# Performance work log

Measured on AMD Instinct MI355X. Metric: run time of the kernel, lower is better.

Reference implementation:

```python
import jax, jax.numpy as jnp
import numpy as np
import math

B, S, E, H = 2, 2048, 1024, 16
D = E // H  # head_dim = 64


def setup_inputs() -> dict:
    key = jax.random.key(0)
    ks = jax.random.split(key, 5)
    scale_p = 1.0 / math.sqrt(D)
    return {
        "x": jax.random.normal(ks[0], (B, S, E), dtype=jnp.float32),
        "Wq": jax.random.normal(ks[1], (D, D), dtype=jnp.float32) * scale_p,
        "Wk": jax.random.normal(ks[2], (D, D), dtype=jnp.float32) * scale_p,
        "Wv": jax.random.normal(ks[3], (D, D), dtype=jnp.float32) * scale_p,
        "W_out": jax.random.normal(ks[4], (E, E), dtype=jnp.float32) * (1.0 / math.sqrt(E)),
        "b_out": jnp.zeros((E,), dtype=jnp.float32),
    }


def reference(x, Wq, Wk, Wv, W_out, b_out):
    b, s, e = x.shape
    xh = x.reshape(b, s, H, D)  # [B,S,H,D]
    # per-head linear projections (torch Linear: y = x @ W.T), weights shared across heads
    q = jnp.einsum("bshd,ed->bshe", xh, Wq)
    k = jnp.einsum("bshd,ed->bshe", xh, Wk)
    v = jnp.einsum("bshd,ed->bshe", xh, Wv)
    # scaled dot-product attention, scale = sqrt(embed_dim) per tutorial-style impl
    energy = jnp.einsum("bqhd,bkhd->bhqk", q, k) / jnp.sqrt(jnp.float32(e))
    attn = jax.nn.softmax(energy, axis=-1)  # [B,H,S,S]
    out = jnp.einsum("bhqk,bkhd->bqhd", attn, v).reshape(b, s, e)
    return out @ W_out.T + b_out
```

## Files before the change

### kernel.cpp

```cpp
#include <hip/hip_runtime.h>
#include <math.h>

#define BB 2
#define SS 2048
#define EE 1024
#define HH 16
#define DD 64
constexpr int NROWS = BB * SS * HH;
constexpr float SCALE_Q = 1.4426950408889634f / 32.0f;

typedef __attribute__((ext_vector_type(8))) short bf16x8;
typedef __attribute__((ext_vector_type(4))) float f32x4;
typedef __attribute__((ext_vector_type(16))) float f32x16;
typedef __attribute__((ext_vector_type(4))) unsigned u32x4;

__device__ inline ushort f2bf(float f) {
  unsigned u = __builtin_bit_cast(unsigned, f);
  u += 0x7fffu + ((u >> 16) & 1u);
  return (ushort)(u >> 16);
}

__device__ inline unsigned cvt_pk(float lo, float hi) {
  unsigned r;
  asm("v_cvt_pk_bf16_f32 %0, %1, %2" : "=v"(r) : "v"(lo), "v"(hi));
  return r;
}

__global__ __launch_bounds__(256) void wqkv_cvt(
    const float* __restrict__ Wq, const float* __restrict__ Wk,
    const float* __restrict__ Wv, ushort* __restrict__ o) {
  int i = blockIdx.x * 256 + threadIdx.x;
  int t = i >> 12, j = i & 4095;
  const float* W = (t == 0) ? Wq : ((t == 1) ? Wk : Wv);
  o[i] = f2bf(W[j]);
}

__global__ __launch_bounds__(256) void qkv_mfma(
    const float* __restrict__ x, const ushort* __restrict__ wqkv,
    ushort* __restrict__ qo, ushort* __restrict__ ko, ushort* __restrict__ vto) {
  __shared__ __align__(16) ushort Xs[128 * 72];
  __shared__ __align__(16) ushort Ws[3][64 * 72];
  const int tid = threadIdx.x, w = tid >> 6, l = tid & 63;
  const int g = l >> 4, c = l & 15;
  const int s0 = blockIdx.x * 128, h = blockIdx.y, b = blockIdx.z;

  for (int i = tid; i < 1536; i += 256) {
    int t = i >> 9, j = i & 511;
    int r = j >> 3, e0 = (j & 7) * 8;
    *(bf16x8*)&Ws[t][r * 72 + e0] = *(const bf16x8*)&wqkv[t * 4096 + r * 64 + e0];
  }
  for (int i = tid; i < 2048; i += 256) {
    int r = i >> 4, c4 = (i & 15) * 4;
    float4 xv = *(const float4*)&x[(((size_t)b * SS + s0 + r) * HH + h) * DD + c4];
    uint2 pk;
    pk.x = cvt_pk(xv.x, xv.y);
    pk.y = cvt_pk(xv.z, xv.w);
    *(uint2*)&Xs[r * 72 + c4] = pk;
  }
  __syncthreads();

  bf16x8 a_[2][2];
#pragma unroll
  for (int rf = 0; rf < 2; ++rf) {
    a_[rf][0] = *(bf16x8*)&Xs[(w * 32 + rf * 16 + c) * 72 + g * 8];
    a_[rf][1] = *(bf16x8*)&Xs[(w * 32 + rf * 16 + c) * 72 + 32 + g * 8];
  }

#pragma unroll
  for (int t = 0; t < 2; ++t) {
    ushort* out = (t == 0) ? qo : ko;
    const float sc = (t == 0) ? SCALE_Q : 1.0f;
#pragma unroll
    for (int ct = 0; ct < 4; ++ct) {
      bf16x8 b0 = *(bf16x8*)&Ws[t][(ct * 16 + c) * 72 + g * 8];
      bf16x8 b1 = *(bf16x8*)&Ws[t][(ct * 16 + c) * 72 + 32 + g * 8];
#pragma unroll
      for (int rf = 0; rf < 2; ++rf) {
        f32x4 acc = (f32x4){0.f, 0.f, 0.f, 0.f};
        acc = __builtin_amdgcn_mfma_f32_16x16x32_bf16(a_[rf][0], b0, acc, 0, 0, 0);
        acc = __builtin_amdgcn_mfma_f32_16x16x32_bf16(a_[rf][1], b1, acc, 0, 0, 0);
#pragma unroll
        for (int r = 0; r < 4; ++r) {
          int srow = w * 32 + rf * 16 + g * 4 + r;
          out[(((size_t)b * SS + s0 + srow) * HH + h) * DD + ct * 16 + c] =
              f2bf(acc[r] * sc);
        }
      }
    }
  }
#pragma unroll
  for (int ct = 0; ct < 4; ++ct) {
    bf16x8 b0 = *(bf16x8*)&Ws[2][(ct * 16 + c) * 72 + g * 8];
    bf16x8 b1 = *(bf16x8*)&Ws[2][(ct * 16 + c) * 72 + 32 + g * 8];
#pragma unroll
    for (int rf = 0; rf < 2; ++rf) {
      f32x4 acc = (f32x4){0.f, 0.f, 0.f, 0.f};
      acc = __builtin_amdgcn_mfma_f32_16x16x32_bf16(a_[rf][0], b0, acc, 0, 0, 0);
      acc = __builtin_amdgcn_mfma_f32_16x16x32_bf16(a_[rf][1], b1, acc, 0, 0, 0);
      uint2 pk;
      pk.x = cvt_pk(acc[0], acc[1]);
      pk.y = cvt_pk(acc[2], acc[3]);
      int d = ct * 16 + c;
      int srow = w * 32 + rf * 16 + g * 4;
      *(uint2*)&vto[(((size_t)b * HH + h) * DD + d) * SS + s0 + srow] = pk;
    }
  }
}

__global__ __launch_bounds__(256) void wcvt(const float* __restrict__ w,
                                            ushort* __restrict__ o) {
  int i = (blockIdx.x * 256 + threadIdx.x) * 8;
  bf16x8 t;
#pragma unroll
  for (int j = 0; j < 8; ++j) t[j] = (short)f2bf(w[i + j]);
  *(bf16x8*)&o[i] = t;
}

__global__ __launch_bounds__(256) void attn_mfma(
    const ushort* __restrict__ q, const ushort* __restrict__ k,
    const ushort* __restrict__ vt, ushort* __restrict__ o) {
  __shared__ __align__(16) ushort Ks[2][64 * 72];
  __shared__ __align__(16) ushort Vts[2][64 * 72];
  const int tid = threadIdx.x, w = tid >> 6, l = tid & 63;
  const int lq = l & 31, h2 = l >> 5;
  const int work = ((blockIdx.x & 7) << 6) | (blockIdx.x >> 3);
  const int qt = work & 15, hb = work >> 4;
  const int h = hb & 15, b = hb >> 4;
  const int q0 = qt * 128;

  const size_t bh_qk = (size_t)b * SS * EE + h * DD;
  const size_t bh_vt = (size_t)b * SS * EE + h * (DD * SS);

  const int sr0 = tid >> 3;
  const int se0 = (tid & 7) * 8;
  const int krow0 = (sr0 & 19) | ((sr0 & 4) << 1) | ((sr0 & 8) >> 1);

  {
    bf16x8 kr0 = *(const bf16x8*)&k[bh_qk + (size_t)sr0 * EE + se0];
    bf16x8 kr1 = *(const bf16x8*)&k[bh_qk + (size_t)(sr0 + 32) * EE + se0];
    bf16x8 vr0 = *(const bf16x8*)&vt[bh_vt + (size_t)sr0 * SS + se0];
    bf16x8 vr1 = *(const bf16x8*)&vt[bh_vt + (size_t)(sr0 + 32) * SS + se0];
    *(bf16x8*)&Ks[0][krow0 * 72 + se0] = kr0;
    *(bf16x8*)&Ks[0][(krow0 + 32) * 72 + se0] = kr1;
    *(bf16x8*)&Vts[0][sr0 * 72 + se0] = vr0;
    *(bf16x8*)&Vts[0][(sr0 + 32) * 72 + se0] = vr1;
  }

  bf16x8 aq[4];
#pragma unroll
  for (int db = 0; db < 4; ++db)
    aq[db] = *(const bf16x8*)&q[bh_qk +
        (size_t)(q0 + w * 32 + lq) * EE + db * 16 + h2 * 8];

  f32x16 accO[2];
  float lacc = 0.f;
#pragma unroll
  for (int ct = 0; ct < 2; ++ct)
#pragma unroll
    for (int r = 0; r < 16; ++r) accO[ct][r] = 0.f;

  __syncthreads();

  for (int t = 0; t < 32; ++t) {
    const int cur = t & 1;
    bf16x8 kr0, kr1, vr0, vr1;
    if (t < 31) {
      const size_t kb2 = bh_qk + (size_t)((t + 1) * 64) * EE;
      kr0 = *(const bf16x8*)&k[kb2 + (size_t)sr0 * EE + se0];
      kr1 = *(const bf16x8*)&k[kb2 + (size_t)(sr0 + 32) * EE + se0];
      const size_t vb2 = bh_vt + (t + 1) * 64;
      vr0 = *(const bf16x8*)&vt[vb2 + (size_t)sr0 * SS + se0];
      vr1 = *(const bf16x8*)&vt[vb2 + (size_t)(sr0 + 32) * SS + se0];
    }

    f32x16 s[2];
    __builtin_amdgcn_s_setprio(1);
#pragma unroll
    for (int kb = 0; kb < 2; ++kb) {
      f32x16 acc;
#pragma unroll
      for (int r = 0; r < 16; ++r) acc[r] = 0.f;
#pragma unroll
      for (int db = 0; db < 4; ++db) {
        bf16x8 ka = *(bf16x8*)&Ks[cur][(kb * 32 + lq) * 72 + db * 16 + h2 * 8];
        acc = __builtin_amdgcn_mfma_f32_32x32x16_bf16(ka, aq[db], acc, 0, 0, 0);
      }
      s[kb] = acc;
    }
    __builtin_amdgcn_s_setprio(0);

    u32x4 pwv[2][2];
#pragma unroll
    for (int kb = 0; kb < 2; ++kb)
#pragma unroll
      for (int t16 = 0; t16 < 2; ++t16)
#pragma unroll
        for (int j2 = 0; j2 < 4; ++j2) {
          float pa = __builtin_amdgcn_exp2f(s[kb][t16 * 8 + j2 * 2]);
          float pb = __builtin_amdgcn_exp2f(s[kb][t16 * 8 + j2 * 2 + 1]);
          lacc += pa + pb;
          pwv[kb][t16][j2] = cvt_pk(pa, pb);
        }

    __builtin_amdgcn_s_setprio(1);
#pragma unroll
    for (int ct = 0; ct < 2; ++ct) {
#pragma unroll
      for (int kb = 0; kb < 2; ++kb)
#pragma unroll
        for (int t16 = 0; t16 < 2; ++t16) {
          bf16x8 va = *(bf16x8*)&Vts[cur][(ct * 32 + lq) * 72 +
                                          kb * 32 + t16 * 16 + h2 * 8];
          accO[ct] = __builtin_amdgcn_mfma_f32_32x32x16_bf16(
              va, __builtin_bit_cast(bf16x8, pwv[kb][t16]), accO[ct], 0, 0, 0);
        }
    }
    __builtin_amdgcn_s_setprio(0);

    if (t < 31) {
      const int nxt = cur ^ 1;
      *(bf16x8*)&Ks[nxt][krow0 * 72 + se0] = kr0;
      *(bf16x8*)&Ks[nxt][(krow0 + 32) * 72 + se0] = kr1;
      *(bf16x8*)&Vts[nxt][sr0 * 72 + se0] = vr0;
      *(bf16x8*)&Vts[nxt][(sr0 + 32) * 72 + se0] = vr1;
    }
    __syncthreads();
  }

  {
    float tsum = lacc + __shfl_xor(lacc, 32, 64);
    float inv = 1.f / tsum;
    size_t row = (size_t)b * SS + q0 + w * 32 + lq;
#pragma unroll
    for (int ct = 0; ct < 2; ++ct)
#pragma unroll
      for (int rq = 0; rq < 4; ++rq) {
        uint2 pk;
        pk.x = cvt_pk(accO[ct][rq * 4 + 0] * inv, accO[ct][rq * 4 + 1] * inv);
        pk.y = cvt_pk(accO[ct][rq * 4 + 2] * inv, accO[ct][rq * 4 + 3] * inv);
        *(uint2*)&o[row * EE + h * DD + ct * 32 + rq * 8 + h2 * 4] = pk;
      }
  }
}

__global__ __launch_bounds__(256) void out_proj_mfma(
    const ushort* __restrict__ a, const ushort* __restrict__ wo,
    const float* __restrict__ bias, float* __restrict__ y) {
  __shared__ __align__(16) ushort As[2][128 * 72];
  __shared__ __align__(16) ushort Ws[2][64 * 72];
  const int tid = threadIdx.x, w = tid >> 6, l = tid & 63;
  const int g = l >> 4, c = l & 15;
  const int m0 = blockIdx.x * 128, n0 = blockIdx.y * 64;
  const int sr = tid >> 3, se = (tid & 7) * 8;

  f32x4 acc[2][4];
#pragma unroll
  for (int mf = 0; mf < 2; ++mf)
#pragma unroll
    for (int ct = 0; ct < 4; ++ct) acc[mf][ct] = (f32x4){0.f, 0.f, 0.f, 0.f};

  {
#pragma unroll
    for (int j = 0; j < 4; ++j) {
      int r = sr + j * 32;
      *(bf16x8*)&As[0][r * 72 + se] = *(const bf16x8*)&a[(size_t)(m0 + r) * EE + se];
    }
#pragma unroll
    for (int j = 0; j < 2; ++j) {
      int r = sr + j * 32;
      *(bf16x8*)&Ws[0][r * 72 + se] = *(const bf16x8*)&wo[(size_t)(n0 + r) * EE + se];
    }
  }
  __syncthreads();

  for (int t = 0; t < 16; ++t) {
    const int cur = t & 1;
    bf16x8 Arg[4], Brg[2];
    if (t < 15) {
      const int k0 = (t + 1) * 64;
#pragma unroll
      for (int j = 0; j < 4; ++j) {
        int r = sr + j * 32;
        Arg[j] = *(const bf16x8*)&a[(size_t)(m0 + r) * EE + k0 + se];
      }
#pragma unroll
      for (int j = 0; j < 2; ++j) {
        int r = sr + j * 32;
        Brg[j] = *(const bf16x8*)&wo[(size_t)(n0 + r) * EE + k0 + se];
      }
    }

    bf16x8 af[2][2];
#pragma unroll
    for (int mf = 0; mf < 2; ++mf) {
      af[mf][0] = *(bf16x8*)&As[cur][(w * 32 + mf * 16 + c) * 72 + g * 8];
      af[mf][1] = *(bf16x8*)&As[cur][(w * 32 + mf * 16 + c) * 72 + 32 + g * 8];
    }
    __builtin_amdgcn_s_setprio(1);
#pragma unroll
    for (int ct = 0; ct < 4; ++ct) {
      bf16x8 b0 = *(bf16x8*)&Ws[cur][(ct * 16 + c) * 72 + g * 8];
      bf16x8 b1 = *(bf16x8*)&Ws[cur][(ct * 16 + c) * 72 + 32 + g * 8];
#pragma unroll
      for (int mf = 0; mf < 2; ++mf) {
        acc[mf][ct] = __builtin_amdgcn_mfma_f32_16x16x32_bf16(af[mf][0], b0, acc[mf][ct], 0, 0, 0);
        acc[mf][ct] = __builtin_amdgcn_mfma_f32_16x16x32_bf16(af[mf][1], b1, acc[mf][ct], 0, 0, 0);
      }
    }
    __builtin_amdgcn_s_setprio(0);

    if (t < 15) {
      const int nxt = cur ^ 1;
#pragma unroll
      for (int j = 0; j < 4; ++j) {
        int r = sr + j * 32;
        *(bf16x8*)&As[nxt][r * 72 + se] = Arg[j];
      }
#pragma unroll
      for (int j = 0; j < 2; ++j) {
        int r = sr + j * 32;
        *(bf16x8*)&Ws[nxt][r * 72 + se] = Brg[j];
      }
    }
    __syncthreads();
  }

#pragma unroll
  for (int ct = 0; ct < 4; ++ct) {
    float bv = bias[n0 + ct * 16 + c];
#pragma unroll
    for (int mf = 0; mf < 2; ++mf)
#pragma unroll
      for (int r = 0; r < 4; ++r)
        y[(size_t)(m0 + w * 32 + mf * 16 + g * 4 + r) * EE + n0 + ct * 16 + c] =
            acc[mf][ct][r] + bv;
  }
}

extern "C" void kernel_launch(void* const* d_in, const int* in_sizes, int n_in,
                              void* d_out, int out_size, void* d_ws,
                              size_t ws_size, hipStream_t stream) {
  const float* x = (const float*)d_in[0];
  const float* Wq = (const float*)d_in[1];
  const float* Wk = (const float*)d_in[2];
  const float* Wv = (const float*)d_in[3];
  const float* Wo = (const float*)d_in[4];
  const float* bo = (const float*)d_in[5];
  float* out = (float*)d_out;

  const size_t per = (size_t)NROWS * 64;
  ushort* qb = (ushort*)d_ws;
  ushort* kb = qb + per;
  ushort* vtb = kb + per;
  ushort* aob = vtb + per;
  ushort* wob = aob + per;
  ushort* wqkvb = wob + 1024 * 1024;

  wqkv_cvt<<<48, 256, 0, stream>>>(Wq, Wk, Wv, wqkvb);
  wcvt<<<512, 256, 0, stream>>>(Wo, wob);
  qkv_mfma<<<dim3(16, 16, 2), 256, 0, stream>>>(x, wqkvb, qb, kb, vtb);
  attn_mfma<<<512, 256, 0, stream>>>(qb, kb, vtb, aob);
  out_proj_mfma<<<dim3(32, 16), 256, 0, stream>>>(aob, wob, bo, out);
}
```

Baseline: 89.75 us.

## Split attention over two key halves with a separate combine kernel

The attention kernel now splits the 2048 keys into two halves handled by separate blocks, doubling the grid to 1024 blocks. Each block writes unnormalized fp32 partial outputs and row sums to workspace instead of a normalized bf16 result. A new combine kernel adds the two partials, divides by the summed row totals and writes the bf16 attention output. This is meant to raise occupancy and latency hiding on the CUs. The cost is a round trip of a large fp32 intermediate through memory plus one extra kernel launch.

```diff
diff --git a/kernel.cpp b/kernel.cpp
--- a/kernel.cpp
+++ b/kernel.cpp
@@ -118,28 +118,34 @@
 
 __global__ __launch_bounds__(256) void attn_mfma(
     const ushort* __restrict__ q, const ushort* __restrict__ k,
-    const ushort* __restrict__ vt, ushort* __restrict__ o) {
+    const ushort* __restrict__ vt, float* __restrict__ pO,
+    float* __restrict__ lsum) {
   __shared__ __align__(16) ushort Ks[2][64 * 72];
   __shared__ __align__(16) ushort Vts[2][64 * 72];
   const int tid = threadIdx.x, w = tid >> 6, l = tid & 63;
   const int lq = l & 31, h2 = l >> 5;
-  const int work = ((blockIdx.x & 7) << 6) | (blockIdx.x >> 3);
-  const int qt = work & 15, hb = work >> 4;
+  const int work = ((blockIdx.x & 7) << 7) | (blockIdx.x >> 3);
+  const int qt = work & 15;
+  const int split = (work >> 4) & 1;
+  const int hb = work >> 5;
   const int h = hb & 15, b = hb >> 4;
   const int q0 = qt * 128;
+  const int k0base = split * 1024;
 
   const size_t bh_qk = (size_t)b * SS * EE + h * DD;
   const size_t bh_vt = (size_t)b * SS * EE + h * (DD * SS);
+  const size_t kq_base = bh_qk + (size_t)k0base * EE;
+  const size_t vt_base = bh_vt + k0base;
 
   const int sr0 = tid >> 3;
   const int se0 = (tid & 7) * 8;
   const int krow0 = (sr0 & 19) | ((sr0 & 4) << 1) | ((sr0 & 8) >> 1);
 
   {
-    bf16x8 kr0 = *(const bf16x8*)&k[bh_qk + (size_t)sr0 * EE + se0];
-    bf16x8 kr1 = *(const bf16x8*)&k[bh_qk + (size_t)(sr0 + 32) * EE + se0];
-    bf16x8 vr0 = *(const bf16x8*)&vt[bh_vt + (size_t)sr0 * SS + se0];
-    bf16x8 vr1 = *(const bf16x8*)&vt[bh_vt + (size_t)(sr0 + 32) * SS + se0];
+    bf16x8 kr0 = *(const bf16x8*)&k[kq_base + (size_t)sr0 * EE + se0];
+    bf16x8 kr1 = *(const bf16x8*)&k[kq_base + (size_t)(sr0 + 32) * EE + se0];
+    bf16x8 vr0 = *(const bf16x8*)&vt[vt_base + (size_t)sr0 * SS + se0];
+    bf16x8 vr1 = *(const bf16x8*)&vt[vt_base + (size_t)(sr0 + 32) * SS + se0];
     *(bf16x8*)&Ks[0][krow0 * 72 + se0] = kr0;
     *(bf16x8*)&Ks[0][(krow0 + 32) * 72 + se0] = kr1;
     *(bf16x8*)&Vts[0][sr0 * 72 + se0] = vr0;
@@ -153,7 +159,7 @@
         (size_t)(q0 + w * 32 + lq) * EE + db * 16 + h2 * 8];
 
   f32x16 accO[2];
-  float lacc = 0.f;
+  float lacc[2] = {0.f, 0.f};
 #pragma unroll
   for (int ct = 0; ct < 2; ++ct)
 #pragma unroll
@@ -161,14 +167,14 @@
 
   __syncthreads();
 
-  for (int t = 0; t < 32; ++t) {
+  for (int t = 0; t < 16; ++t) {
     const int cur = t & 1;
     bf16x8 kr0, kr1, vr0, vr1;
-    if (t < 31) {
-      const size_t kb2 = bh_qk + (size_t)((t + 1) * 64) * EE;
+    if (t < 15) {
+      const size_t kb2 = kq_base + (size_t)((t + 1) * 64) * EE;
       kr0 = *(const bf16x8*)&k[kb2 + (size_t)sr0 * EE + se0];
       kr1 = *(const bf16x8*)&k[kb2 + (size_t)(sr0 + 32) * EE + se0];
-      const size_t vb2 = bh_vt + (t + 1) * 64;
+      const size_t vb2 = vt_base + (t + 1) * 64;
       vr0 = *(const bf16x8*)&vt[vb2 + (size_t)sr0 * SS + se0];
       vr1 = *(const bf16x8*)&vt[vb2 + (size_t)(sr0 + 32) * SS + se0];
     }
@@ -198,7 +204,7 @@
         for (int j2 = 0; j2 < 4; ++j2) {
           float pa = __builtin_amdgcn_exp2f(s[kb][t16 * 8 + j2 * 2]);
           float pb = __builtin_amdgcn_exp2f(s[kb][t16 * 8 + j2 * 2 + 1]);
-          lacc += pa + pb;
+          lacc[kb] += pa + pb;
           pwv[kb][t16][j2] = cvt_pk(pa, pb);
         }
 
@@ -217,7 +223,7 @@
     }
     __builtin_amdgcn_s_setprio(0);
 
-    if (t < 31) {
+    if (t < 15) {
       const int nxt = cur ^ 1;
       *(bf16x8*)&Ks[nxt][krow0 * 72 + se0] = kr0;
       *(bf16x8*)&Ks[nxt][(krow0 + 32) * 72 + se0] = kr1;
@@ -228,18 +234,44 @@
   }
 
   {
-    float tsum = lacc + __shfl_xor(lacc, 32, 64);
-    float inv = 1.f / tsum;
-    size_t row = (size_t)b * SS + q0 + w * 32 + lq;
+    float tsum = lacc[0] + lacc[1];
+    tsum += __shfl_xor(tsum, 32, 64);
+    const int qrow = q0 + w * 32 + lq;
+    if (h2 == 0)
+      lsum[((size_t)split * BB * HH + (size_t)b * HH + h) * SS + qrow] = tsum;
+    float* dst = pO + (size_t)split * NROWS * 64 +
+                 ((size_t)b * SS + qrow) * EE + h * DD;
 #pragma unroll
     for (int ct = 0; ct < 2; ++ct)
 #pragma unroll
       for (int rq = 0; rq < 4; ++rq) {
-        uint2 pk;
-        pk.x = cvt_pk(accO[ct][rq * 4 + 0] * inv, accO[ct][rq * 4 + 1] * inv);
-        pk.y = cvt_pk(accO[ct][rq * 4 + 2] * inv, accO[ct][rq * 4 + 3] * inv);
-        *(uint2*)&o[row * EE + h * DD + ct * 32 + rq * 8 + h2 * 4] = pk;
-      }
+        float4 v4 = {accO[ct][rq * 4 + 0], accO[ct][rq * 4 + 1],
+                     accO[ct][rq * 4 + 2], accO[ct][rq * 4 + 3]};
+        *(float4*)&dst[ct * 32 + rq * 8 + h2 * 4] = v4;
+      }
+  }
+}
+
+__global__ __launch_bounds__(256) void attn_combine(
+    const float* __restrict__ pO, const float* __restrict__ lsum,
+    ushort* __restrict__ o) {
+  const int gid = blockIdx.x * 256 + threadIdx.x;
+#pragma unroll
+  for (int j = 0; j < 2; ++j) {
+    const int idx = gid * 2 + j;
+    const int e4 = idx * 4;
+    const int row = e4 >> 10;
+    const int e = e4 & 1023;
+    const int h = e >> 6;
+    const int b = row >> 11, s = row & 2047;
+    float4 a0 = *(const float4*)&pO[e4];
+    float4 a1 = *(const float4*)&pO[(size_t)NROWS * 64 + e4];
+    const size_t li = ((size_t)b * HH + h) * SS + s;
+    float inv = 1.f / (lsum[li] + lsum[(size_t)BB * HH * SS + li]);
+    uint2 pk;
+    pk.x = cvt_pk((a0.x + a1.x) * inv, (a0.y + a1.y) * inv);
+    pk.y = cvt_pk((a0.z + a1.z) * inv, (a0.w + a1.w) * inv);
+    *(uint2*)&o[e4] = pk;
   }
 }
 
@@ -355,10 +387,13 @@
   ushort* aob = vtb + per;
   ushort* wob = aob + per;
   ushort* wqkvb = wob + 1024 * 1024;
+  float* pO = (float*)(wqkvb + 16384);
+  float* lsum = pO + 2 * per;
 
   wqkv_cvt<<<48, 256, 0, stream>>>(Wq, Wk, Wv, wqkvb);
   wcvt<<<512, 256, 0, stream>>>(Wo, wob);
   qkv_mfma<<<dim3(16, 16, 2), 256, 0, stream>>>(x, wqkvb, qb, kb, vtb);
-  attn_mfma<<<512, 256, 0, stream>>>(qb, kb, vtb, aob);
+  attn_mfma<<<1024, 256, 0, stream>>>(qb, kb, vtb, pO, lsum);
+  attn_combine<<<2048, 256, 0, stream>>>(pO, lsum, aob);
   out_proj_mfma<<<dim3(32, 16), 256, 0, stream>>>(aob, wob, bo, out);
 }
```

Result: slower. 98.44 us (+9.7%).

## Load K/V MFMA fragments directly from global into registers, drop LDS staging

Applied to the files above, without the earlier changes.

The attention kernel no longer stages K and V tiles through double-buffered shared memory with block-wide barriers. Each wave now loads its MFMA operand fragments straight from global memory into registers, prefetching the next K tile into a ping-pong register set and loading V fragments at the start of each iteration. This removes the LDS writes, LDS reads and __syncthreads per tile. In exchange, all four waves in a block fetch the same K/V data separately, so global/L2 traffic rises, V loads are exposed within the iteration, and register pressure grows.

```diff
diff --git a/kernel.cpp b/kernel.cpp
--- a/kernel.cpp
+++ b/kernel.cpp
@@ -119,59 +119,54 @@
 __global__ __launch_bounds__(256) void attn_mfma(
     const ushort* __restrict__ q, const ushort* __restrict__ k,
     const ushort* __restrict__ vt, ushort* __restrict__ o) {
-  __shared__ __align__(16) ushort Ks[2][64 * 72];
-  __shared__ __align__(16) ushort Vts[2][64 * 72];
   const int tid = threadIdx.x, w = tid >> 6, l = tid & 63;
   const int lq = l & 31, h2 = l >> 5;
   const int work = ((blockIdx.x & 7) << 6) | (blockIdx.x >> 3);
   const int qt = work & 15, hb = work >> 4;
   const int h = hb & 15, b = hb >> 4;
-  const int q0 = qt * 128;
+  const int q0 = qt * 128 + w * 32;
 
   const size_t bh_qk = (size_t)b * SS * EE + h * DD;
   const size_t bh_vt = (size_t)b * SS * EE + h * (DD * SS);
 
-  const int sr0 = tid >> 3;
-  const int se0 = (tid & 7) * 8;
-  const int krow0 = (sr0 & 19) | ((sr0 & 4) << 1) | ((sr0 & 8) >> 1);
-
+  const int ksig = (lq & 19) | ((lq & 4) << 1) | ((lq & 8) >> 1);
+  const ushort* kbase = k + bh_qk + (size_t)ksig * EE + h2 * 8;
+  const ushort* vbase = vt + bh_vt + (size_t)lq * SS + h2 * 8;
+
+  bf16x8 aq[4];
+#pragma unroll
+  for (int db = 0; db < 4; ++db)
+    aq[db] = *(const bf16x8*)&q[bh_qk + (size_t)(q0 + lq) * EE + db * 16 + h2 * 8];
+
+  f32x16 accO[2];
+  float lacc[2] = {0.f, 0.f};
+#pragma unroll
+  for (int ct = 0; ct < 2; ++ct)
+#pragma unroll
+    for (int r = 0; r < 16; ++r) accO[ct][r] = 0.f;
+
+  bf16x8 kfA[8], kfB[8];
   {
-    bf16x8 kr0 = *(const bf16x8*)&k[bh_qk + (size_t)sr0 * EE + se0];
-    bf16x8 kr1 = *(const bf16x8*)&k[bh_qk + (size_t)(sr0 + 32) * EE + se0];
-    bf16x8 vr0 = *(const bf16x8*)&vt[bh_vt + (size_t)sr0 * SS + se0];
-    bf16x8 vr1 = *(const bf16x8*)&vt[bh_vt + (size_t)(sr0 + 32) * SS + se0];
-    *(bf16x8*)&Ks[0][krow0 * 72 + se0] = kr0;
-    *(bf16x8*)&Ks[0][(krow0 + 32) * 72 + se0] = kr1;
-    *(bf16x8*)&Vts[0][sr0 * 72 + se0] = vr0;
-    *(bf16x8*)&Vts[0][(sr0 + 32) * 72 + se0] = vr1;
-  }
-
-  bf16x8 aq[4];
-#pragma unroll
-  for (int db = 0; db < 4; ++db)
-    aq[db] = *(const bf16x8*)&q[bh_qk +
-        (size_t)(q0 + w * 32 + lq) * EE + db * 16 + h2 * 8];
-
-  f32x16 accO[2];
-  float lacc = 0.f;
-#pragma unroll
-  for (int ct = 0; ct < 2; ++ct)
-#pragma unroll
-    for (int r = 0; r < 16; ++r) accO[ct][r] = 0.f;
-
-  __syncthreads();
-
-  for (int t = 0; t < 32; ++t) {
-    const int cur = t & 1;
-    bf16x8 kr0, kr1, vr0, vr1;
-    if (t < 31) {
-      const size_t kb2 = bh_qk + (size_t)((t + 1) * 64) * EE;
-      kr0 = *(const bf16x8*)&k[kb2 + (size_t)sr0 * EE + se0];
-      kr1 = *(const bf16x8*)&k[kb2 + (size_t)(sr0 + 32) * EE + se0];
-      const size_t vb2 = bh_vt + (t + 1) * 64;
-      vr0 = *(const bf16x8*)&vt[vb2 + (size_t)sr0 * SS + se0];
-      vr1 = *(const bf16x8*)&vt[vb2 + (size_t)(sr0 + 32) * SS + se0];
-    }
+    const ushort* ka0 = kbase;
+    const ushort* ka1 = kbase + (size_t)32 * EE;
+#pragma unroll
+    for (int db = 0; db < 4; ++db) {
+      kfA[db] = *(const bf16x8*)&ka0[db * 16];
+      kfA[4 + db] = *(const bf16x8*)&ka1[db * 16];
+    }
+  }
+
+  auto body = [&](int tt, bf16x8 (&kcur)[8], bf16x8 (&knxt)[8]) {
+    bf16x8 vf[8];
+    const ushort* va0 = vbase + tt * 64;
+    const ushort* va1 = va0 + (size_t)32 * SS;
+#pragma unroll
+    for (int kb = 0; kb < 2; ++kb)
+#pragma unroll
+      for (int t16 = 0; t16 < 2; ++t16) {
+        vf[kb * 2 + t16] = *(const bf16x8*)&va0[kb * 32 + t16 * 16];
+        vf[4 + kb * 2 + t16] = *(const bf16x8*)&va1[kb * 32 + t16 * 16];
+      }
 
     f32x16 s[2];
     __builtin_amdgcn_s_setprio(1);
@@ -181,13 +176,23 @@
 #pragma unroll
       for (int r = 0; r < 16; ++r) acc[r] = 0.f;
 #pragma unroll
+      for (int db = 0; db < 4; ++db)
+        acc = __builtin_amdgcn_mfma_f32_32x32x16_bf16(kcur[kb * 4 + db], aq[db],
+                                                      acc, 0, 0, 0);
+      s[kb] = acc;
+    }
+    __builtin_amdgcn_s_setprio(0);
+
+    {
+      const int tn = (tt + 1) & 31;
+      const ushort* ka0 = kbase + (size_t)(tn * 64) * EE;
+      const ushort* ka1 = ka0 + (size_t)32 * EE;
+#pragma unroll
       for (int db = 0; db < 4; ++db) {
-        bf16x8 ka = *(bf16x8*)&Ks[cur][(kb * 32 + lq) * 72 + db * 16 + h2 * 8];
-        acc = __builtin_amdgcn_mfma_f32_32x32x16_bf16(ka, aq[db], acc, 0, 0, 0);
-      }
-      s[kb] = acc;
-    }
-    __builtin_amdgcn_s_setprio(0);
+        knxt[db] = *(const bf16x8*)&ka0[db * 16];
+        knxt[4 + db] = *(const bf16x8*)&ka1[db * 16];
+      }
+    }
 
     u32x4 pwv[2][2];
 #pragma unroll
@@ -198,39 +203,33 @@
         for (int j2 = 0; j2 < 4; ++j2) {
           float pa = __builtin_amdgcn_exp2f(s[kb][t16 * 8 + j2 * 2]);
           float pb = __builtin_amdgcn_exp2f(s[kb][t16 * 8 + j2 * 2 + 1]);
-          lacc += pa + pb;
+          lacc[kb] += pa + pb;
           pwv[kb][t16][j2] = cvt_pk(pa, pb);
         }
 
     __builtin_amdgcn_s_setprio(1);
 #pragma unroll
-    for (int ct = 0; ct < 2; ++ct) {
+    for (int ct = 0; ct < 2; ++ct)
 #pragma unroll
       for (int kb = 0; kb < 2; ++kb)
 #pragma unroll
-        for (int t16 = 0; t16 < 2; ++t16) {
-          bf16x8 va = *(bf16x8*)&Vts[cur][(ct * 32 + lq) * 72 +
-                                          kb * 32 + t16 * 16 + h2 * 8];
+        for (int t16 = 0; t16 < 2; ++t16)
           accO[ct] = __builtin_amdgcn_mfma_f32_32x32x16_bf16(
-              va, __builtin_bit_cast(bf16x8, pwv[kb][t16]), accO[ct], 0, 0, 0);
-        }
-    }
+              vf[ct * 4 + kb * 2 + t16],
+              __builtin_bit_cast(bf16x8, pwv[kb][t16]), accO[ct], 0, 0, 0);
     __builtin_amdgcn_s_setprio(0);
-
-    if (t < 31) {
-      const int nxt = cur ^ 1;
-      *(bf16x8*)&Ks[nxt][krow0 * 72 + se0] = kr0;
-      *(bf16x8*)&Ks[nxt][(krow0 + 32) * 72 + se0] = kr1;
-      *(bf16x8*)&Vts[nxt][sr0 * 72 + se0] = vr0;
-      *(bf16x8*)&Vts[nxt][(sr0 + 32) * 72 + se0] = vr1;
-    }
-    __syncthreads();
+  };
+
+  for (int t = 0; t < 32; t += 2) {
+    body(t, kfA, kfB);
+    body(t + 1, kfB, kfA);
   }
 
   {
-    float tsum = lacc + __shfl_xor(lacc, 32, 64);
+    float tsum = lacc[0] + lacc[1];
+    tsum += __shfl_xor(tsum, 32, 64);
     float inv = 1.f / tsum;
-    size_t row = (size_t)b * SS + q0 + w * 32 + lq;
+    size_t row = (size_t)b * SS + q0 + lq;
 #pragma unroll
     for (int ct = 0; ct < 2; ++ct)
 #pragma unroll
```

Result: slower. 160.3 us (+78.6%).

## Double query rows per wave in attention and merge weight conversion kernels

Applied to the files above, without the earlier changes.

The attention kernel now gives each wave 64 query rows instead of 32, so each block covers 256 queries. K and V fragments loaded from LDS are reused across two query sub-tiles, and the grid drops from 512 to 256 blocks with launch_bounds(256,1). The two weight-conversion kernels are merged into one vectorized kernel to save a launch. The trade-off is higher register pressure and only 256 blocks, which may underfill the 256 CUs on MI355X.

```diff
diff --git a/kernel.cpp b/kernel.cpp
--- a/kernel.cpp
+++ b/kernel.cpp
@@ -26,13 +26,31 @@
   return r;
 }
 
-__global__ __launch_bounds__(256) void wqkv_cvt(
+__global__ __launch_bounds__(256) void wconv(
     const float* __restrict__ Wq, const float* __restrict__ Wk,
-    const float* __restrict__ Wv, ushort* __restrict__ o) {
-  int i = blockIdx.x * 256 + threadIdx.x;
-  int t = i >> 12, j = i & 4095;
-  const float* W = (t == 0) ? Wq : ((t == 1) ? Wk : Wv);
-  o[i] = f2bf(W[j]);
+    const float* __restrict__ Wv, const float* __restrict__ Wo,
+    ushort* __restrict__ wqkvb, ushort* __restrict__ wob) {
+  int idx = blockIdx.x * 256 + threadIdx.x;
+  const float* sp;
+  ushort* dp;
+  if (idx < 1536) {
+    int t = idx >> 9, j = idx & 511;
+    const float* W = (t == 0) ? Wq : ((t == 1) ? Wk : Wv);
+    sp = W + j * 8;
+    dp = wqkvb + t * 4096 + j * 8;
+  } else {
+    size_t j = (size_t)(idx - 1536) * 8;
+    sp = Wo + j;
+    dp = wob + j;
+  }
+  float4 a = *(const float4*)sp;
+  float4 c = *(const float4*)(sp + 4);
+  u32x4 r;
+  r[0] = cvt_pk(a.x, a.y);
+  r[1] = cvt_pk(a.z, a.w);
+  r[2] = cvt_pk(c.x, c.y);
+  r[3] = cvt_pk(c.z, c.w);
+  *(u32x4*)dp = r;
 }
 
 __global__ __launch_bounds__(256) void qkv_mfma(
@@ -107,26 +125,17 @@
   }
 }
 
-__global__ __launch_bounds__(256) void wcvt(const float* __restrict__ w,
-                                            ushort* __restrict__ o) {
-  int i = (blockIdx.x * 256 + threadIdx.x) * 8;
-  bf16x8 t;
-#pragma unroll
-  for (int j = 0; j < 8; ++j) t[j] = (short)f2bf(w[i + j]);
-  *(bf16x8*)&o[i] = t;
-}
-
-__global__ __launch_bounds__(256) void attn_mfma(
+__global__ __launch_bounds__(256, 1) void attn_mfma(
     const ushort* __restrict__ q, const ushort* __restrict__ k,
     const ushort* __restrict__ vt, ushort* __restrict__ o) {
   __shared__ __align__(16) ushort Ks[2][64 * 72];
   __shared__ __align__(16) ushort Vts[2][64 * 72];
   const int tid = threadIdx.x, w = tid >> 6, l = tid & 63;
   const int lq = l & 31, h2 = l >> 5;
-  const int work = ((blockIdx.x & 7) << 6) | (blockIdx.x >> 3);
-  const int qt = work & 15, hb = work >> 4;
+  const int work = ((blockIdx.x & 7) << 5) | (blockIdx.x >> 3);
+  const int qt = work & 7, hb = work >> 3;
   const int h = hb & 15, b = hb >> 4;
-  const int q0 = qt * 128;
+  const int q0 = qt * 256 + w * 64;
 
   const size_t bh_qk = (size_t)b * SS * EE + h * DD;
   const size_t bh_vt = (size_t)b * SS * EE + h * (DD * SS);
@@ -146,18 +155,25 @@
     *(bf16x8*)&Vts[0][(sr0 + 32) * 72 + se0] = vr1;
   }
 
-  bf16x8 aq[4];
-#pragma unroll
-  for (int db = 0; db < 4; ++db)
-    aq[db] = *(const bf16x8*)&q[bh_qk +
-        (size_t)(q0 + w * 32 + lq) * EE + db * 16 + h2 * 8];
-
-  f32x16 accO[2];
-  float lacc = 0.f;
-#pragma unroll
-  for (int ct = 0; ct < 2; ++ct)
-#pragma unroll
-    for (int r = 0; r < 16; ++r) accO[ct][r] = 0.f;
+  bf16x8 aq[2][4];
+#pragma unroll
+  for (int qb = 0; qb < 2; ++qb)
+#pragma unroll
+    for (int db = 0; db < 4; ++db)
+      aq[qb][db] = *(const bf16x8*)&q[bh_qk +
+          (size_t)(q0 + qb * 32 + lq) * EE + db * 16 + h2 * 8];
+
+  f32x16 accO[2][2];
+  float lacc[2][2];
+#pragma unroll
+  for (int qb = 0; qb < 2; ++qb) {
+    lacc[qb][0] = 0.f;
+    lacc[qb][1] = 0.f;
+#pragma unroll
+    for (int ct = 0; ct < 2; ++ct)
+#pragma unroll
+      for (int r = 0; r < 16; ++r) accO[qb][ct][r] = 0.f;
+  }
 
   __syncthreads();
 
@@ -173,48 +189,67 @@
       vr1 = *(const bf16x8*)&vt[vb2 + (size_t)(sr0 + 32) * SS + se0];
     }
 
-    f32x16 s[2];
+    bf16x8 kf[2][4];
+#pragma unroll
+    for (int kb = 0; kb < 2; ++kb)
+#pragma unroll
+      for (int db = 0; db < 4; ++db)
+        kf[kb][db] = *(bf16x8*)&Ks[cur][(kb * 32 + lq) * 72 + db * 16 + h2 * 8];
+
+    u32x4 pwv[2][2][2];
+#pragma unroll
+    for (int qb = 0; qb < 2; ++qb) {
+      f32x16 s[2];
+      __builtin_amdgcn_s_setprio(1);
+#pragma unroll
+      for (int kb = 0; kb < 2; ++kb) {
+        f32x16 acc;
+#pragma unroll
+        for (int r = 0; r < 16; ++r) acc[r] = 0.f;
+#pragma unroll
+        for (int db = 0; db < 4; ++db)
+          acc = __builtin_amdgcn_mfma_f32_32x32x16_bf16(kf[kb][db], aq[qb][db],
+                                                        acc, 0, 0, 0);
+        s[kb] = acc;
+      }
+      __builtin_amdgcn_s_setprio(0);
+#pragma unroll
+      for (int kb = 0; kb < 2; ++kb)
+#pragma unroll
+        for (int t16 = 0; t16 < 2; ++t16)
+#pragma unroll
+          for (int j2 = 0; j2 < 4; ++j2) {
+            float pa = __builtin_amdgcn_exp2f(s[kb][t16 * 8 + j2 * 2]);
+            float pb = __builtin_amdgcn_exp2f(s[kb][t16 * 8 + j2 * 2 + 1]);
+            lacc[qb][kb] += pa + pb;
+            pwv[qb][kb][t16][j2] = cvt_pk(pa, pb);
+          }
+    }
+
+    bf16x8 vf[2][4];
+#pragma unroll
+    for (int ct = 0; ct < 2; ++ct)
+#pragma unroll
+      for (int kb = 0; kb < 2; ++kb)
+#pragma unroll
+        for (int t16 = 0; t16 < 2; ++t16)
+          vf[ct][kb * 2 + t16] = *(bf16x8*)&Vts[cur][(ct * 32 + lq) * 72 +
+                                                     kb * 32 + t16 * 16 + h2 * 8];
+
     __builtin_amdgcn_s_setprio(1);
 #pragma unroll
-    for (int kb = 0; kb < 2; ++kb) {
-      f32x16 acc;
-#pragma unroll
-      for (int r = 0; r < 16; ++r) acc[r] = 0.f;
-#pragma unroll
-      for (int db = 0; db < 4; ++db) {
-        bf16x8 ka = *(bf16x8*)&Ks[cur][(kb * 32 + lq) * 72 + db * 16 + h2 * 8];
-        acc = __builtin_amdgcn_mfma_f32_32x32x16_bf16(ka, aq[db], acc, 0, 0, 0);
-      }
-      s[kb] = acc;
-    }
-    __builtin_amdgcn_s_setprio(0);
-
-    u32x4 pwv[2][2];
-#pragma unroll
-    for (int kb = 0; kb < 2; ++kb)
-#pragma unroll
-      for (int t16 = 0; t16 < 2; ++t16)
-#pragma unroll
-        for (int j2 = 0; j2 < 4; ++j2) {
-          float pa = __builtin_amdgcn_exp2f(s[kb][t16 * 8 + j2 * 2]);
-          float pb = __builtin_amdgcn_exp2f(s[kb][t16 * 8 + j2 * 2 + 1]);
-          lacc += pa + pb;
-          pwv[kb][t16][j2] = cvt_pk(pa, pb);
+    for (int ct = 0; ct < 2; ++ct)
+#pragma unroll
+      for (int kb = 0; kb < 2; ++kb)
+#pragma unroll
+        for (int t16 = 0; t16 < 2; ++t16) {
+          accO[0][ct] = __builtin_amdgcn_mfma_f32_32x32x16_bf16(
+              vf[ct][kb * 2 + t16],
+              __builtin_bit_cast(bf16x8, pwv[0][kb][t16]), accO[0][ct], 0, 0, 0);
+          accO[1][ct] = __builtin_amdgcn_mfma_f32_32x32x16_bf16(
+              vf[ct][kb * 2 + t16],
+              __builtin_bit_cast(bf16x8, pwv[1][kb][t16]), accO[1][ct], 0, 0, 0);
         }
-
-    __builtin_amdgcn_s_setprio(1);
-#pragma unroll
-    for (int ct = 0; ct < 2; ++ct) {
-#pragma unroll
-      for (int kb = 0; kb < 2; ++kb)
-#pragma unroll
-        for (int t16 = 0; t16 < 2; ++t16) {
-          bf16x8 va = *(bf16x8*)&Vts[cur][(ct * 32 + lq) * 72 +
-                                          kb * 32 + t16 * 16 + h2 * 8];
-          accO[ct] = __builtin_amdgcn_mfma_f32_32x32x16_bf16(
-              va, __builtin_bit_cast(bf16x8, pwv[kb][t16]), accO[ct], 0, 0, 0);
-        }
-    }
     __builtin_amdgcn_s_setprio(0);
 
     if (t < 31) {
@@ -227,17 +262,21 @@
     __syncthreads();
   }
 
-  {
-    float tsum = lacc + __shfl_xor(lacc, 32, 64);
+#pragma unroll
+  for (int qb = 0; qb < 2; ++qb) {
+    float tsum = lacc[qb][0] + lacc[qb][1];
+    tsum += __shfl_xor(tsum, 32, 64);
     float inv = 1.f / tsum;
-    size_t row = (size_t)b * SS + q0 + w * 32 + lq;
+    size_t row = (size_t)b * SS + q0 + qb * 32 + lq;
 #pragma unroll
     for (int ct = 0; ct < 2; ++ct)
 #pragma unroll
       for (int rq = 0; rq < 4; ++rq) {
         uint2 pk;
-        pk.x = cvt_pk(accO[ct][rq * 4 + 0] * inv, accO[ct][rq * 4 + 1] * inv);
-        pk.y = cvt_pk(accO[ct][rq * 4 + 2] * inv, accO[ct][rq * 4 + 3] * inv);
+        pk.x = cvt_pk(accO[qb][ct][rq * 4 + 0] * inv,
+                      accO[qb][ct][rq * 4 + 1] * inv);
+        pk.y = cvt_pk(accO[qb][ct][rq * 4 + 2] * inv,
+                      accO[qb][ct][rq * 4 + 3] * inv);
         *(uint2*)&o[row * EE + h * DD + ct * 32 + rq * 8 + h2 * 4] = pk;
       }
   }
@@ -356,9 +395,8 @@
   ushort* wob = aob + per;
   ushort* wqkvb = wob + 1024 * 1024;
 
-  wqkv_cvt<<<48, 256, 0, stream>>>(Wq, Wk, Wv, wqkvb);
-  wcvt<<<512, 256, 0, stream>>>(Wo, wob);
+  wconv<<<518, 256, 0, stream>>>(Wq, Wk, Wv, Wo, wqkvb, wob);
   qkv_mfma<<<dim3(16, 16, 2), 256, 0, stream>>>(x, wqkvb, qb, kb, vtb);
-  attn_mfma<<<512, 256, 0, stream>>>(qb, kb, vtb, aob);
+  attn_mfma<<<256, 256, 0, stream>>>(qb, kb, vtb, aob);
   out_proj_mfma<<<dim3(32, 16), 256, 0, stream>>>(aob, wob, bo, out);
 }
```

After: 87.44 us. 2.6% less time.
